# Performance work log

Hardware: AMD Instinct MI355X
Metric: run time of the kernel (lower is better)

## Reference

```python
import math
import jax, jax.numpy as jnp
import numpy as np

NUM_EXPERTS = 8
TOP_K = 2
HIDDEN = 1024
INTER = 4096
CAPACITY_FACTOR = 1.25
S, B = 2048, 4


def setup_inputs() -> dict:
    key = jax.random.key(0)
    k1, k2, k3, k4 = jax.random.split(key, 4)
    hidden_states = jax.random.normal(k1, (S, B, HIDDEN), dtype=jnp.float32)
    T = S * B
    logits = jax.random.normal(k2, (T, NUM_EXPERTS), dtype=jnp.float32)
    expert_affinities = jax.nn.softmax(logits, axis=-1)  # (T, E), normalized per token
    # top-k chosen experts per token (no duplicates), consistent with affinities
    _, expert_index = jax.lax.top_k(expert_affinities, TOP_K)  # (T, top_k) int32
    gate_up_proj = jax.random.normal(k3, (NUM_EXPERTS, HIDDEN, 2 * INTER), dtype=jnp.float32) * 0.02
    down_proj = jax.random.normal(k4, (NUM_EXPERTS, INTER, HIDDEN), dtype=jnp.float32) * 0.02
    return {
        "hidden_states": hidden_states,
        "expert_affinities": expert_affinities,
        "expert_index": expert_index.astype(jnp.int32),
        "gate_up_proj": gate_up_proj,
        "down_proj": down_proj,
    }


def reference(hidden_states, expert_affinities, expert_index, gate_up_proj, down_proj):
    S_, B_, H = hidden_states.shape
    T = S_ * B_
    E = expert_affinities.shape[1]
    K = expert_index.shape[1]
    # expert capacity (static, as in compute_position_in_expert)
    C = min(math.ceil(T * K * CAPACITY_FACTOR / E), T)

    x = hidden_states.reshape(T, H)

    # top_k-hot expert mask (T, E)
    expert_mask = jnp.sum(jax.nn.one_hot(expert_index, E, dtype=jnp.int32), axis=1)
    # 1-indexed position of each token within each chosen expert
    position_in_expert = jnp.cumsum(expert_mask, axis=0) * expert_mask  # (T, E)
    kept = (expert_mask > 0) & (position_in_expert <= C)  # capacity drop
    pos0 = position_in_expert - 1  # 0-indexed

    # gather per-(token, k) positions / keep flags
    pos_tk = jnp.take_along_axis(pos0, expert_index, axis=1)          # (T, K)
    kept_tk = jnp.take_along_axis(kept, expert_index, axis=1)         # (T, K)
    flat_idx = jnp.where(kept_tk, expert_index * C + pos_tk, E * C)   # dropped -> dummy slot

    # dispatch: scatter tokens into per-expert buffers (E*C [+1 dummy], H)
    src = jnp.broadcast_to(x[:, None, :], (T, K, H)).reshape(T * K, H)
    dispatched = jnp.zeros((E * C + 1, H), dtype=x.dtype).at[flat_idx.reshape(-1)].add(src)
    expert_buf = dispatched[: E * C].reshape(E, C, H)

    # grouped expert MLP (GLU): gate/up projection, SiLU gating, down projection
    gate_up = jnp.einsum("ech,ehf->ecf", expert_buf, gate_up_proj)    # (E, C, 2I)
    gate, up = jnp.split(gate_up, 2, axis=2)
    intermediate = jax.nn.silu(gate) * up                              # (E, C, I)
    expert_out = jnp.einsum("eci,eih->ech", intermediate, down_proj)   # (E, C, H)

    # combine: gather each token's expert outputs, weight by (normalized) affinities
    out_flat = jnp.concatenate(
        [expert_out.reshape(E * C, H), jnp.zeros((1, H), dtype=expert_out.dtype)], axis=0
    )
    aff_tk = jnp.take_along_axis(expert_affinities, expert_index, axis=1)  # (T, K)
    aff_tk = aff_tk / jnp.sum(aff_tk, axis=-1, keepdims=True)  # normalize_top_k_affinities
    weights = aff_tk * kept_tk.astype(aff_tk.dtype)            # dropped tokens contribute 0
    tok_out = jnp.sum(out_flat[flat_idx] * weights[..., None], axis=1)  # (T, H)
    return tok_out.reshape(S_, B_, H)
```

## Files before the change

### kernel.cpp

```cpp
#include <hip/hip_runtime.h>
#include <hip/hip_bf16.h>

#define NE 8
#define HID 1024
#define INT_ 4096
#define NTOK 8192
#define CAP 2560

typedef short short8 __attribute__((ext_vector_type(8)));
typedef float floatx4 __attribute__((ext_vector_type(4)));

__device__ __forceinline__ unsigned short f2bf(float f) {
  union { float f; unsigned int u; } v; v.f = f;
  unsigned int u = v.u;
  return (unsigned short)((u + 0x7fffu + ((u >> 16) & 1u)) >> 16);
}

__device__ __forceinline__ void gl2lds16(const void* g, void* l) {
  __builtin_amdgcn_global_load_lds(
      (const __attribute__((address_space(1))) unsigned int*)g,
      (__attribute__((address_space(3))) unsigned int*)l, 16, 0, 0);
}

__global__ void routing_kernel(const int* __restrict__ eidx,
                               int* __restrict__ tfs,
                               int* __restrict__ counts, int* __restrict__ slots) {
  __shared__ unsigned long long masks[128];
  __shared__ int ccnt[128];
  int e = blockIdx.x;
  int tid = threadIdx.x;
  int wave = tid >> 6, lane = tid & 63;

  for (int ch = wave; ch < 128; ch += 4) {
    int t = ch * 64 + lane;
    int2 pr = ((const int2*)eidx)[t];
    bool chosen = (pr.x == e) || (pr.y == e);
    unsigned long long m = __ballot(chosen);
    if (lane == 0) { masks[ch] = m; ccnt[ch] = __popcll(m); }
  }
  __syncthreads();
  if (tid == 0) {
    int run = 0;
    for (int i = 0; i < 128; ++i) { int c = ccnt[i]; ccnt[i] = run; run += c; }
    counts[e] = run < CAP ? run : CAP;
  }
  __syncthreads();
  for (int ch = wave; ch < 128; ch += 4) {
    int t = ch * 64 + lane;
    unsigned long long m = masks[ch];
    if ((m >> lane) & 1ull) {
      int pos = ccnt[ch] + __popcll(m & ((2ull << lane) - 1ull));
      int2 pr = ((const int2*)eidx)[t];
      int kk = (pr.x == e) ? 0 : 1;
      if (pos <= CAP) {
        int slot = e * CAP + pos - 1;
        tfs[slot] = t;
        slots[2 * t + kk] = slot;
      } else {
        slots[2 * t + kk] = -1;
      }
    }
  }
}

__global__ void transpose_cvt_kernel(const float* __restrict__ in, unsigned short* __restrict__ out,
                                     int R, int Cc) {
  __shared__ unsigned short tile[64 * 66];
  int z = blockIdx.z;
  int r0 = blockIdx.y * 64, c0 = blockIdx.x * 64;
  const float* inp = in + (size_t)z * R * Cc;
  unsigned short* outp = out + (size_t)z * R * Cc;
  int tx = threadIdx.x & 15, ty = threadIdx.x >> 4;
#pragma unroll
  for (int j = 0; j < 4; ++j) {
    int r = ty + j * 16;
    float4 v = *(const float4*)(inp + (size_t)(r0 + r) * Cc + c0 + 4 * tx);
    tile[r * 66 + 4 * tx + 0] = f2bf(v.x);
    tile[r * 66 + 4 * tx + 1] = f2bf(v.y);
    tile[r * 66 + 4 * tx + 2] = f2bf(v.z);
    tile[r * 66 + 4 * tx + 3] = f2bf(v.w);
  }
  __syncthreads();
#pragma unroll
  for (int j = 0; j < 4; ++j) {
    int c = ty + j * 16;
    ushort4 p;
    p.x = tile[(4 * tx + 0) * 66 + c];
    p.y = tile[(4 * tx + 1) * 66 + c];
    p.z = tile[(4 * tx + 2) * 66 + c];
    p.w = tile[(4 * tx + 3) * 66 + c];
    *(ushort4*)(outp + (size_t)(c0 + c) * R + r0 + 4 * tx) = p;
  }
}

__global__ void dispatch_kernel(const float* __restrict__ x, const int* __restrict__ tfs,
                                const int* __restrict__ counts, unsigned short* __restrict__ ebuf) {
  int slot = blockIdx.x;
  int e = slot / CAP, c = slot - e * CAP;
  bool valid = c < counts[e];
  int t = valid ? tfs[slot] : 0;
  const float4* src = (const float4*)(x + (size_t)t * HID);
  ushort4* dst = (ushort4*)(ebuf + (size_t)slot * HID);
#pragma unroll
  for (int j = 0; j < 2; ++j) {
    int i = threadIdx.x + j * 128;
    ushort4 p;
    if (valid) {
      float4 v = src[i];
      p.x = f2bf(v.x); p.y = f2bf(v.y); p.z = f2bf(v.z); p.w = f2bf(v.w);
    } else {
      p.x = p.y = p.z = p.w = 0;
    }
    dst[i] = p;
  }
}


#define BARX() do { asm volatile("" ::: "memory"); __builtin_amdgcn_s_barrier(); \
  __builtin_amdgcn_sched_barrier(0); asm volatile("" ::: "memory"); } while (0)
#define VMW4() asm volatile("s_waitcnt vmcnt(4)" ::: "memory")

#define STAGE_A(SBUF, HALF, KT) do { \
  _Pragma("unroll") for (int rr = 0; rr < 2; ++rr) { \
    int lrow_ = (HALF) * 128 + rr * 64 + (tid >> 3); \
    int gk_ = (KT) + (((tid & 7) ^ (lrow_ & 7)) << 3); \
    gl2lds16(Ab + (size_t)lrow_ * KD + gk_, \
             (SBUF) + ((HALF) * 128 + rr * 64 + wave * 8) * 64); \
  } } while (0)

#define STAGE_B(SBUF, HALF, KT) do { \
  _Pragma("unroll") for (int rr = 0; rr < 2; ++rr) { \
    int sr_ = rr * 64 + (tid >> 3); \
    int gk_ = (KT) + (((tid & 7) ^ (sr_ & 7)) << 3); \
    gl2lds16(((HALF) ? Bb1 : Bb0) + (size_t)sr_ * KD + gk_, \
             (SBUF) + 16384 + ((HALF) * 128 + rr * 64 + wave * 8) * 64); \
  } } while (0)

#define LDA_Q(SBUF, QM) do { \
  _Pragma("unroll") for (int ml = 0; ml < 4; ++ml) { \
    int rA_ = (QM) * 128 + w_m * 64 + ml * 16 + rl; \
    _Pragma("unroll") for (int ks = 0; ks < 2; ++ks) { \
      int pc_ = (ks * 4 + quad) ^ (rA_ & 7); \
      a[ml][ks] = *(const short8*)((SBUF) + rA_ * 64 + pc_ * 8); \
    } } } while (0)

#define LDB_Q(SBUF, QN, BREG) do { \
  _Pragma("unroll") for (int nl = 0; nl < 2; ++nl) { \
    int rB_ = (QN) * 128 + w_n * 32 + nl * 16 + rl; \
    _Pragma("unroll") for (int ks = 0; ks < 2; ++ks) { \
      int pc_ = (ks * 4 + quad) ^ (rB_ & 7); \
      BREG[nl][ks] = *(const short8*)((SBUF) + 16384 + rB_ * 64 + pc_ * 8); \
    } } } while (0)

#define MFMA_Q(QM, QN, BREG) do { \
  __builtin_amdgcn_s_setprio(1); \
  _Pragma("unroll") for (int ml = 0; ml < 4; ++ml) \
    _Pragma("unroll") for (int nl = 0; nl < 2; ++nl) \
      _Pragma("unroll") for (int ks = 0; ks < 2; ++ks) \
        acc[(QM) * 4 + ml][(QN) * 2 + nl] = __builtin_amdgcn_mfma_f32_16x16x32_bf16( \
            a[ml][ks], BREG[nl][ks], acc[(QM) * 4 + ml][(QN) * 2 + nl], 0, 0, 0); \
  __builtin_amdgcn_s_setprio(0); \
} while (0)

template <int KD, bool GLU>
__global__ __launch_bounds__(512, 2) void gemm256_kernel(
    const unsigned short* __restrict__ A, const unsigned short* __restrict__ B,
    const int* __restrict__ counts, unsigned short* __restrict__ obf,
    float* __restrict__ of) {
  int gx = gridDim.x, gy = gridDim.y;
  int h = blockIdx.x + gx * (blockIdx.y + gy * blockIdx.z);
  int nwg = gx * gy * (int)gridDim.z;
  int wg = (h & 7) * (nwg >> 3) + (h >> 3);
  int e = wg / (gx * gy);
  int rem = wg - e * (gx * gy);
  int bxi = rem / gy;
  int byi = rem - bxi * gy;

  int c0 = byi * 256;
  if (c0 >= counts[e]) return;

  __shared__ alignas(16) unsigned short smem[65536];
  unsigned short* s0 = smem;
  unsigned short* s1 = smem + 32768;

  int tid = threadIdx.x;
  int wave = tid >> 6, lane = tid & 63;
  int w_m = wave >> 2, w_n = wave & 3;
  int rl = lane & 15, quad = lane >> 4;

  const unsigned short* Ab = A + ((size_t)e * CAP + c0) * KD;
  const unsigned short* Bb0;
  const unsigned short* Bb1;
  int n0;
  if constexpr (GLU) {
    n0 = bxi * 128;
    Bb0 = B + ((size_t)e * 2 * INT_ + n0) * KD;
    Bb1 = B + ((size_t)e * 2 * INT_ + INT_ + n0) * KD;
  } else {
    n0 = bxi * 256;
    Bb0 = B + ((size_t)e * HID + n0) * KD;
    Bb1 = Bb0 + (size_t)128 * KD;
  }

  short8 a[4][2], b0[2][2], b1[2][2];
  floatx4 acc[8][4];
#pragma unroll
  for (int i = 0; i < 8; ++i)
#pragma unroll
    for (int j = 0; j < 4; ++j) acc[i][j] = (floatx4){0.f, 0.f, 0.f, 0.f};

  STAGE_A(s0, 0, 0);
  STAGE_B(s0, 0, 0);
  STAGE_B(s0, 1, 0);
  STAGE_A(s0, 1, 0);
  VMW4();
  BARX();

  for (int it = 0; it < KD / 128; ++it) {
    int kt1 = it * 128 + 64;
    int ktn = (it * 128 + 128 < KD) ? (it * 128 + 128) : 0;
    LDA_Q(s0, 0);
    LDB_Q(s0, 0, b0);
    STAGE_A(s1, 0, kt1);
    VMW4(); BARX();
    MFMA_Q(0, 0, b0);
    LDB_Q(s0, 1, b1);
    STAGE_B(s1, 0, kt1);
    VMW4(); BARX();
    MFMA_Q(0, 1, b1);
    LDA_Q(s0, 1);
    STAGE_B(s1, 1, kt1);
    BARX();
    MFMA_Q(1, 1, b1);
    STAGE_A(s1, 1, kt1);
    VMW4(); BARX();
    MFMA_Q(1, 0, b0);
    LDA_Q(s1, 0);
    LDB_Q(s1, 0, b0);
    STAGE_A(s0, 0, ktn);
    VMW4(); BARX();
    MFMA_Q(0, 0, b0);
    LDB_Q(s1, 1, b1);
    STAGE_B(s0, 0, ktn);
    VMW4(); BARX();
    MFMA_Q(0, 1, b1);
    LDA_Q(s1, 1);
    STAGE_B(s0, 1, ktn);
    BARX();
    MFMA_Q(1, 1, b1);
    STAGE_A(s0, 1, ktn);
    VMW4(); BARX();
    MFMA_Q(1, 0, b0);
  }
  asm volatile("s_waitcnt vmcnt(0)" ::: "memory");

#pragma unroll
  for (int mi = 0; mi < 8; ++mi) {
    int row = (mi >> 2) * 128 + w_m * 64 + (mi & 3) * 16 + quad * 4;
    if constexpr (GLU) {
#pragma unroll
      for (int nl = 0; nl < 2; ++nl) {
        int col = n0 + w_n * 32 + nl * 16 + rl;
#pragma unroll
        for (int r = 0; r < 4; ++r) {
          float g = acc[mi][nl][r];
          float u = acc[mi][nl + 2][r];
          float s = g / (1.f + __expf(-g));
          obf[((size_t)e * CAP + c0 + row + r) * INT_ + col] = f2bf(s * u);
        }
      }
    } else {
#pragma unroll
      for (int ni = 0; ni < 4; ++ni) {
        int col = n0 + (ni >> 1) * 128 + w_n * 32 + (ni & 1) * 16 + rl;
#pragma unroll
        for (int r = 0; r < 4; ++r)
          of[((size_t)e * CAP + c0 + row + r) * HID + col] = acc[mi][ni][r];
      }
    }
  }
}

__global__ void combine_kernel(const float4* __restrict__ eout, const int* __restrict__ slots,
                               const float* __restrict__ aff, const int* __restrict__ eidx,
                               float4* __restrict__ out) {
  int t = blockIdx.x;
  int i = threadIdx.x;
  int s0 = slots[2 * t], s1 = slots[2 * t + 1];
  int e0 = eidx[2 * t], e1 = eidx[2 * t + 1];
  float a0 = aff[t * NE + e0], a1 = aff[t * NE + e1];
  float inv = 1.f / (a0 + a1);
  float w0 = (s0 >= 0) ? a0 * inv : 0.f;
  float w1 = (s1 >= 0) ? a1 * inv : 0.f;
  int p0 = (s0 >= 0) ? s0 : 0;
  int p1 = (s1 >= 0) ? s1 : 0;
  float4 v0 = eout[(size_t)p0 * 256 + i];
  float4 v1 = eout[(size_t)p1 * 256 + i];
  float4 r;
  r.x = w0 * v0.x + w1 * v1.x;
  r.y = w0 * v0.y + w1 * v1.y;
  r.z = w0 * v0.z + w1 * v1.z;
  r.w = w0 * v0.w + w1 * v1.w;
  out[(size_t)t * 256 + i] = r;
}

extern "C" void kernel_launch(void* const* d_in, const int* in_sizes, int n_in,
                              void* d_out, int out_size, void* d_ws, size_t ws_size,
                              hipStream_t stream) {
  const float* x = (const float*)d_in[0];
  const float* aff = (const float*)d_in[1];
  const int* eidx = (const int*)d_in[2];
  const float* wgu_f = (const float*)d_in[3];
  const float* wd_f = (const float*)d_in[4];
  float* out = (float*)d_out;

  char* ws = (char*)d_ws;
  int* tfs = (int*)(ws + 0);
  int* counts = (int*)(ws + 163840);
  int* slots = (int*)(ws + 196608);
  unsigned short* ebuf = (unsigned short*)(ws + 262144);
  unsigned short* wgu = (unsigned short*)(ws + 42205184);
  unsigned short* wd = (unsigned short*)(ws + 176422912);
  unsigned short* inter = (unsigned short*)(ws + 243531776);
  float* eout = (float*)(ws + 42205184);

  routing_kernel<<<NE, 256, 0, stream>>>(eidx, tfs, counts, slots);
  transpose_cvt_kernel<<<dim3(128, 16, NE), 256, 0, stream>>>(wgu_f, wgu, 1024, 8192);
  transpose_cvt_kernel<<<dim3(16, 64, NE), 256, 0, stream>>>(wd_f, wd, 4096, 1024);
  dispatch_kernel<<<NE * CAP, 128, 0, stream>>>(x, tfs, counts, ebuf);
  gemm256_kernel<HID, true><<<dim3(32, 10, NE), 512, 0, stream>>>(
      ebuf, wgu, counts, inter, (float*)nullptr);
  gemm256_kernel<INT_, false><<<dim3(4, 10, NE), 512, 0, stream>>>(
      inter, wd, counts, (unsigned short*)nullptr, eout);
  combine_kernel<<<NTOK, 256, 0, stream>>>((const float4*)eout, slots, aff, eidx, (float4*)out);
}
```

Measured before the change: 1.005 ms.

## Deepen GEMM prefetch pipeline and split barriers around MFMA phases

Restructures the MFMA main loop so global-to-LDS staging runs about one extra quarter-tile further ahead: the prologue issues most of the second buffer, and the wait allows more outstanding loads (vmcnt 10 instead of 4). Each phase is now framed by a barrier plus an LDS-read drain before the MFMA block and a second barrier after it. The aim is to hide more global memory latency behind compute. In exchange there are twice as many barriers per phase, and the reordered stage/read sequence must stay race-free on the two LDS buffers.

```diff
diff --git a/kernel.cpp b/kernel.cpp
--- a/kernel.cpp
+++ b/kernel.cpp
@@ -116,9 +116,19 @@
 }
 
 
-#define BARX() do { asm volatile("" ::: "memory"); __builtin_amdgcn_s_barrier(); \
-  __builtin_amdgcn_sched_barrier(0); asm volatile("" ::: "memory"); } while (0)
-#define VMW4() asm volatile("s_waitcnt vmcnt(4)" ::: "memory")
+#define PH_SYNC() do { \
+  asm volatile("s_waitcnt vmcnt(10)" ::: "memory"); \
+  __builtin_amdgcn_sched_barrier(0); \
+  __builtin_amdgcn_s_barrier(); \
+  asm volatile("s_waitcnt lgkmcnt(0)" ::: "memory"); \
+  __builtin_amdgcn_sched_barrier(0); \
+} while (0)
+
+#define PH_END() do { \
+  __builtin_amdgcn_sched_barrier(0); \
+  __builtin_amdgcn_s_barrier(); \
+  __builtin_amdgcn_sched_barrier(0); \
+} while (0)
 
 #define STAGE_A(SBUF, HALF, KT) do { \
   _Pragma("unroll") for (int rr = 0; rr < 2; ++rr) { \
@@ -213,44 +223,40 @@
   STAGE_B(s0, 0, 0);
   STAGE_B(s0, 1, 0);
   STAGE_A(s0, 1, 0);
-  VMW4();
-  BARX();
+  STAGE_A(s1, 0, 64);
+  STAGE_B(s1, 0, 64);
+  STAGE_B(s1, 1, 64);
+  asm volatile("s_waitcnt vmcnt(10)" ::: "memory");
+  __builtin_amdgcn_sched_barrier(0);
+  __builtin_amdgcn_s_barrier();
+  __builtin_amdgcn_sched_barrier(0);
 
   for (int it = 0; it < KD / 128; ++it) {
-    int kt1 = it * 128 + 64;
-    int ktn = (it * 128 + 128 < KD) ? (it * 128 + 128) : 0;
-    LDA_Q(s0, 0);
-    LDB_Q(s0, 0, b0);
-    STAGE_A(s1, 0, kt1);
-    VMW4(); BARX();
-    MFMA_Q(0, 0, b0);
+    int ktb = it * 128 + 64;
+    int tc = it * 128 + 128; int ktc = (tc < KD) ? tc : 0;
+    int td = it * 128 + 192; int ktd = (td < KD) ? td : 0;
+    LDA_Q(s0, 0); LDB_Q(s0, 0, b0);
+    STAGE_A(s1, 1, ktb);
+    PH_SYNC(); MFMA_Q(0, 0, b0); PH_END();
     LDB_Q(s0, 1, b1);
-    STAGE_B(s1, 0, kt1);
-    VMW4(); BARX();
-    MFMA_Q(0, 1, b1);
+    STAGE_A(s0, 0, ktc);
+    PH_SYNC(); MFMA_Q(0, 1, b1); PH_END();
     LDA_Q(s0, 1);
-    STAGE_B(s1, 1, kt1);
-    BARX();
-    MFMA_Q(1, 1, b1);
-    STAGE_A(s1, 1, kt1);
-    VMW4(); BARX();
-    MFMA_Q(1, 0, b0);
-    LDA_Q(s1, 0);
-    LDB_Q(s1, 0, b0);
-    STAGE_A(s0, 0, ktn);
-    VMW4(); BARX();
-    MFMA_Q(0, 0, b0);
+    STAGE_B(s0, 0, ktc);
+    PH_SYNC(); MFMA_Q(1, 1, b1); PH_END();
+    STAGE_B(s0, 1, ktc);
+    PH_SYNC(); MFMA_Q(1, 0, b0); PH_END();
+    LDA_Q(s1, 0); LDB_Q(s1, 0, b0);
+    STAGE_A(s0, 1, ktc);
+    PH_SYNC(); MFMA_Q(0, 0, b0); PH_END();
     LDB_Q(s1, 1, b1);
-    STAGE_B(s0, 0, ktn);
-    VMW4(); BARX();
-    MFMA_Q(0, 1, b1);
+    STAGE_A(s1, 0, ktd);
+    PH_SYNC(); MFMA_Q(0, 1, b1); PH_END();
     LDA_Q(s1, 1);
-    STAGE_B(s0, 1, ktn);
-    BARX();
-    MFMA_Q(1, 1, b1);
-    STAGE_A(s0, 1, ktn);
-    VMW4(); BARX();
-    MFMA_Q(1, 0, b0);
+    STAGE_B(s1, 0, ktd);
+    PH_SYNC(); MFMA_Q(1, 1, b1); PH_END();
+    STAGE_B(s1, 1, ktd);
+    PH_SYNC(); MFMA_Q(1, 0, b0); PH_END();
   }
   asm volatile("s_waitcnt vmcnt(0)" ::: "memory");
 
```

Result: slower. 1.033 ms (+2.8%).
